# Kernel tuning notes

Hardware: AMD Instinct MI355X
Metric: run time of the kernel (lower is better)

Reference implementation:

```python
import jax, jax.numpy as jnp
import numpy as np

B, L, K, NR, S = 512, 1024, 8, 512, 20  # batch, seq_len, n_matrices, n_rates, alphabet
EXT = 26  # extended alphabet (20 std aa + 6 special), pad of 6 in call()


def _expm(A):
    """Differentiable matrix exponential for small batched matrices (..., n, n).
    Scaling-and-squaring with an order-16 Taylor series (fixed 6 squarings).
    Matches tf.linalg.expm to high accuracy for the small-norm tau*Q here."""
    SQ = 6
    A = A / jnp.asarray(2.0 ** SQ, A.dtype)
    n = A.shape[-1]
    I = jnp.eye(n, dtype=A.dtype)
    P = I + A
    T = A
    for i in range(2, 17):
        T = jnp.matmul(T, A) / i
        P = P + T
    for _ in range(SQ):
        P = jnp.matmul(P, P)
    return P


def setup_inputs() -> dict:
    key = jax.random.key(0)
    k1, k2, k3, k4, k5 = jax.random.split(key, 5)
    return {
        "inputs": jax.random.randint(k1, (B, L), 0, EXT, dtype=jnp.int32),
        "rate_indices": jax.random.randint(k2, (B,), 0, NR, dtype=jnp.int32),
        "tau_kernel": jax.random.normal(k3, (NR,), dtype=jnp.float32),
        "exchangeability_kernel": jax.random.normal(k4, (K, S, S), dtype=jnp.float32),
        "frequencies": jax.random.uniform(k5, (S,), dtype=jnp.float32, minval=0.01, maxval=1.0),
    }


def reference(inputs, rate_indices, tau_kernel, exchangeability_kernel, frequencies):
    b, l = inputs.shape
    mask = inputs < S                                   # (b, L) std-aa mask
    std = jnp.where(mask, inputs, 0)                    # clamp special tokens to 0
    maskf = mask.astype(jnp.float32)[:, :, None, None]  # (b, L, 1, 1)

    # make_R: symmetrize, softplus, zero diagonal
    eye = jnp.eye(S, dtype=jnp.float32)
    R = jax.nn.softplus(0.5 * (exchangeability_kernel + jnp.swapaxes(exchangeability_kernel, -1, -2)))
    R = R * (1.0 - eye)

    # make_rate_matrix: Q = R * pi, subtract row-sum diagonal, normalize by expected rate
    Q = R * frequencies[None, None, :]                  # (k, s, s)
    diag = jnp.sum(Q, axis=-1, keepdims=True)           # (k, s, 1)
    Q = Q - diag * eye
    mue = jnp.sum(frequencies[None, :, None] * diag, axis=-2, keepdims=True)  # (k, 1, 1)
    Q = Q / jnp.maximum(mue, 1e-16)

    # per-sequence evolutionary times
    tau = jax.nn.softplus(tau_kernel)[rate_indices]     # (b,)

    # batched small-matrix expm: (b, k, s, s)
    P = _expm(tau[:, None, None, None] * Q[None])

    # gather ancestral probability rows: (b, L, k, s)
    anc = P[jnp.arange(b)[:, None], :, std, :]
    anc = anc * maskf
    anc = jnp.pad(anc, ((0, 0), (0, 0), (0, 0), (0, EXT - S)))  # pad 20 -> 26
    rest = jax.nn.one_hot(inputs, EXT, dtype=jnp.float32)[:, :, None, :] * (1.0 - maskf)
    anc = anc + rest                                    # (b, L, k, 26)
    return anc.reshape(b, l, -1)                        # (b, L, k*26)
```

## Files before the change

### kernel.cpp

```cpp
#include <hip/hip_runtime.h>
#include <math.h>

#define B    512
#define L    1024
#define K    8
#define NR   512
#define S    20
#define EXT  26
#define SS   (S*S)
#define PD   24
#define PDSQ (PD*PD)
#define ROWF (K*EXT)
#define BROW (L*ROWF)

__device__ __forceinline__ float softplusf(float x) {
    return fmaxf(x, 0.0f) + log1pf(expf(-fabsf(x)));
}

__device__ __forceinline__ void wave_fence() {
    __builtin_amdgcn_wave_barrier();
}

__global__ __launch_bounds__(512, 2) void fused_kernel(
    const int*   __restrict__ inputs,
    const int*   __restrict__ rate_indices,
    const float* __restrict__ tau_kernel,
    const float* __restrict__ exch,
    const float* __restrict__ freq,
    float* __restrict__ out)
{
    __shared__ __align__(16) float M[K][2][PDSQ];
    __shared__ __align__(16) float Row[EXT*ROWF];
    __shared__ int   inp_sh[L];
    __shared__ float diag_sh[K][S];
    __shared__ float mue_sh[K];

    const int b    = blockIdx.x;
    const int t    = threadIdx.x;
    const int w    = t >> 6;
    const int lane = t & 63;
    const int li = lane >> 3, lj = lane & 7;
    const int r0 = 3*li, c0 = 3*lj;

    for (int u = t; u < L; u += 512) inp_sh[u] = inputs[b*L + u];
    for (int e = t; e < EXT*ROWF; e += 512) {
        int row = e / ROWF, c = e - row*ROWF;
        int k = c / EXT, s = c - k*EXT;
        if (row < S) {
            if (s >= S) Row[e] = 0.f;
        } else {
            Row[e] = (s == row) ? 1.f : 0.f;
        }
    }
    float* M0 = &M[w][0][0];
    float* M1 = &M[w][1][0];
    for (int e = lane; e < 2*PDSQ; e += 64) M0[e] = 0.f;
    float tau = softplusf(tau_kernel[rate_indices[b]]);
    wave_fence();

    const float* E = exch + w * SS;
    for (int e = lane; e < SS; e += 64) {
        int r = e / S, c = e - r*S;
        float v = 0.f;
        if (r != c)
            v = softplusf(0.5f * (E[r*S + c] + E[c*S + r])) * freq[c];
        M0[r*PD + c] = v;
    }
    wave_fence();
    if (lane < S) {
        float d = 0.f;
        #pragma unroll
        for (int j = 0; j < S; ++j) d += M0[lane*PD + j];
        diag_sh[w][lane] = d;
    }
    wave_fence();
    if (lane == 0) {
        float m = 0.f;
        #pragma unroll
        for (int s = 0; s < S; ++s) m += freq[s] * diag_sh[w][s];
        mue_sh[w] = fmaxf(m, 1e-16f);
    }
    wave_fence();
    {
        float scale = tau * 0.015625f;
        float mue   = mue_sh[w];
        for (int e = lane; e < SS; e += 64) {
            int r = e / S, c = e - r*S;
            float v = (r == c) ? -diag_sh[w][r] : M0[r*PD + c];
            M0[r*PD + c] = (v / mue) * scale;
        }
    }
    wave_fence();

    float Ac[S][3];
    #pragma unroll
    for (int j = 0; j < S; ++j) {
        #pragma unroll
        for (int d = 0; d < 3; ++d)
            Ac[j][d] = M0[j*PD + c0 + d];
    }

    float P[3][3];
    #pragma unroll
    for (int dr = 0; dr < 3; ++dr)
        #pragma unroll
        for (int dc = 0; dc < 3; ++dc) {
            int r = r0 + dr, c = c0 + dc;
            P[dr][dc] = M0[r*PD + c] + ((r == c && r < S) ? 1.f : 0.f);
        }

    const float* Tc = M0;
    float* Tn = M1;
    #pragma unroll 1
    for (int i = 2; i <= 10; ++i) {
        float C[3][3] = {{0.f,0.f,0.f},{0.f,0.f,0.f},{0.f,0.f,0.f}};
        #pragma unroll
        for (int jc = 0; jc < 5; ++jc) {
            float4 a0 = *(const float4*)&Tc[(r0+0)*PD + 4*jc];
            float4 a1 = *(const float4*)&Tc[(r0+1)*PD + 4*jc];
            float4 a2 = *(const float4*)&Tc[(r0+2)*PD + 4*jc];
            float t0[4] = {a0.x, a0.y, a0.z, a0.w};
            float t1[4] = {a1.x, a1.y, a1.z, a1.w};
            float t2[4] = {a2.x, a2.y, a2.z, a2.w};
            #pragma unroll
            for (int dj = 0; dj < 4; ++dj) {
                int j = 4*jc + dj;
                #pragma unroll
                for (int dc = 0; dc < 3; ++dc) {
                    C[0][dc] = fmaf(t0[dj], Ac[j][dc], C[0][dc]);
                    C[1][dc] = fmaf(t1[dj], Ac[j][dc], C[1][dc]);
                    C[2][dc] = fmaf(t2[dj], Ac[j][dc], C[2][dc]);
                }
            }
        }
        float inv = 1.0f / (float)i;
        #pragma unroll
        for (int dr = 0; dr < 3; ++dr)
            #pragma unroll
            for (int dc = 0; dc < 3; ++dc) {
                C[dr][dc] *= inv;
                P[dr][dc] += C[dr][dc];
                Tn[(r0+dr)*PD + c0 + dc] = C[dr][dc];
            }
        wave_fence();
        float* tmp = (float*)Tc; Tc = Tn; Tn = tmp;
    }

    #pragma unroll 1
    for (int sq = 0; sq < 6; ++sq) {
        #pragma unroll
        for (int dr = 0; dr < 3; ++dr)
            #pragma unroll
            for (int dc = 0; dc < 3; ++dc)
                Tn[(r0+dr)*PD + c0 + dc] = P[dr][dc];
        wave_fence();
        const float* Pb = Tn;
        float C[3][3] = {{0.f,0.f,0.f},{0.f,0.f,0.f},{0.f,0.f,0.f}};
        #pragma unroll
        for (int jc = 0; jc < 5; ++jc) {
            float4 a0 = *(const float4*)&Pb[(r0+0)*PD + 4*jc];
            float4 a1 = *(const float4*)&Pb[(r0+1)*PD + 4*jc];
            float4 a2 = *(const float4*)&Pb[(r0+2)*PD + 4*jc];
            float t0[4] = {a0.x, a0.y, a0.z, a0.w};
            float t1[4] = {a1.x, a1.y, a1.z, a1.w};
            float t2[4] = {a2.x, a2.y, a2.z, a2.w};
            float cb[4][3];
            #pragma unroll
            for (int dj = 0; dj < 4; ++dj)
                #pragma unroll
                for (int dc = 0; dc < 3; ++dc)
                    cb[dj][dc] = Pb[(4*jc + dj)*PD + c0 + dc];
            #pragma unroll
            for (int dj = 0; dj < 4; ++dj)
                #pragma unroll
                for (int dc = 0; dc < 3; ++dc) {
                    C[0][dc] = fmaf(t0[dj], cb[dj][dc], C[0][dc]);
                    C[1][dc] = fmaf(t1[dj], cb[dj][dc], C[1][dc]);
                    C[2][dc] = fmaf(t2[dj], cb[dj][dc], C[2][dc]);
                }
        }
        #pragma unroll
        for (int dr = 0; dr < 3; ++dr)
            #pragma unroll
            for (int dc = 0; dc < 3; ++dc)
                P[dr][dc] = C[dr][dc];
        float* tmp = (float*)Tc; Tc = Tn; Tn = tmp;
        wave_fence();
    }

    #pragma unroll
    for (int dr = 0; dr < 3; ++dr) {
        int r = r0 + dr; if (r >= S) continue;
        #pragma unroll
        for (int dc = 0; dc < 3; ++dc) {
            int c = c0 + dc; if (c >= S) continue;
            Row[r*ROWF + w*EXT + c] = P[dr][dc];
        }
    }
    __syncthreads();

    int l0[13], qq[13];
    {
        int uu = t;
        #pragma unroll
        for (int j = 0; j < 13; ++j) {
            l0[j] = uu / 52;
            qq[j] = uu - l0[j] * 52;
            uu += 512;
        }
    }
    const float4* Row4 = (const float4*)Row;
    float4* out4 = (float4*)out + (size_t)b * (BROW/4);
    #pragma unroll 1
    for (int i = 0; i < 8; ++i) {
        int lbase = i << 7;
        int ubase = t + i * 6656;
        #pragma unroll
        for (int j = 0; j < 13; ++j) {
            int inp = inp_sh[l0[j] + lbase];
            out4[ubase + (j << 9)] = Row4[inp * 52 + qq[j]];
        }
    }
}

extern "C" void kernel_launch(void* const* d_in, const int* in_sizes, int n_in,
                              void* d_out, int out_size, void* d_ws, size_t ws_size,
                              hipStream_t stream) {
    const int*   inputs  = (const int*)  d_in[0];
    const int*   rate_ix = (const int*)  d_in[1];
    const float* tau_k   = (const float*)d_in[2];
    const float* exch    = (const float*)d_in[3];
    const float* freq    = (const float*)d_in[4];
    float* out = (float*)d_out;

    (void)d_ws; (void)ws_size;

    fused_kernel<<<B, 512, 0, stream>>>(inputs, rate_ix, tau_k, exch, freq, out);
}
```

Measured before the change: 478.0 us.

## Split expm and output streaming into two kernels with global LUT and nontemporal stores

The fused kernel becomes two kernels. The first computes the per-batch expm and writes a 26x208 lookup table to workspace. The second kernel runs 2048 blocks of 256 threads, each streaming a quarter of a sequence's output by gathering rows from the global LUT and writing them with nontemporal stores. This is meant to decouple the expm compute from the bandwidth-bound write phase and give the write phase higher occupancy, at the cost of an extra launch and LUT reads that go through L2 instead of LDS.

After: 492.2 us. 3.0% more time.

```diff
diff --git a/kernel.cpp b/kernel.cpp
--- a/kernel.cpp
+++ b/kernel.cpp
@@ -11,7 +11,10 @@
 #define PD   24
 #define PDSQ (PD*PD)
 #define ROWF (K*EXT)
+#define ROWQ ((EXT*ROWF)/4)
 #define BROW (L*ROWF)
+
+typedef float f4 __attribute__((ext_vector_type(4)));
 
 __device__ __forceinline__ float softplusf(float x) {
     return fmaxf(x, 0.0f) + log1pf(expf(-fabsf(x)));
@@ -21,17 +24,15 @@
     __builtin_amdgcn_wave_barrier();
 }
 
-__global__ __launch_bounds__(512, 2) void fused_kernel(
-    const int*   __restrict__ inputs,
+__global__ __launch_bounds__(512, 2) void expm_kernel(
     const int*   __restrict__ rate_indices,
     const float* __restrict__ tau_kernel,
     const float* __restrict__ exch,
     const float* __restrict__ freq,
-    float* __restrict__ out)
+    float*       __restrict__ lut)
 {
     __shared__ __align__(16) float M[K][2][PDSQ];
     __shared__ __align__(16) float Row[EXT*ROWF];
-    __shared__ int   inp_sh[L];
     __shared__ float diag_sh[K][S];
     __shared__ float mue_sh[K];
 
@@ -42,10 +43,10 @@
     const int li = lane >> 3, lj = lane & 7;
     const int r0 = 3*li, c0 = 3*lj;
 
-    for (int u = t; u < L; u += 512) inp_sh[u] = inputs[b*L + u];
     for (int e = t; e < EXT*ROWF; e += 512) {
         int row = e / ROWF, c = e - row*ROWF;
         int k = c / EXT, s = c - k*EXT;
+        (void)k;
         if (row < S) {
             if (s >= S) Row[e] = 0.f;
         } else {
@@ -199,6 +200,25 @@
     }
     __syncthreads();
 
+    f4* dst = (f4*)lut + (size_t)b * ROWQ;
+    const f4* src = (const f4*)Row;
+    for (int e = t; e < ROWQ; e += 512) dst[e] = src[e];
+}
+
+__global__ __launch_bounds__(256, 4) void stream_kernel(
+    const int*   __restrict__ inputs,
+    const float* __restrict__ lut,
+    float*       __restrict__ out)
+{
+    __shared__ int inp_sh[256];
+    const int bid = blockIdx.x;
+    const int b   = bid & (B - 1);
+    const int q   = bid >> 9;
+    const int t   = threadIdx.x;
+
+    inp_sh[t] = inputs[b*L + (q << 8) + t];
+    __syncthreads();
+
     int l0[13], qq[13];
     {
         int uu = t;
@@ -206,19 +226,22 @@
         for (int j = 0; j < 13; ++j) {
             l0[j] = uu / 52;
             qq[j] = uu - l0[j] * 52;
-            uu += 512;
-        }
-    }
-    const float4* Row4 = (const float4*)Row;
-    float4* out4 = (float4*)out + (size_t)b * (BROW/4);
+            uu += 256;
+        }
+    }
+
+    const f4* lut4 = (const f4*)lut + b * ROWQ;
+    f4* out4 = (f4*)out + (size_t)b * (BROW/4) + q * 13312;
+
     #pragma unroll 1
-    for (int i = 0; i < 8; ++i) {
-        int lbase = i << 7;
-        int ubase = t + i * 6656;
+    for (int a = 0; a < 4; ++a) {
+        int lb = a << 6;
+        int ub = t + a * 3328;
         #pragma unroll
         for (int j = 0; j < 13; ++j) {
-            int inp = inp_sh[l0[j] + lbase];
-            out4[ubase + (j << 9)] = Row4[inp * 52 + qq[j]];
+            int inp = inp_sh[l0[j] + lb];
+            f4 v = lut4[inp * 52 + qq[j]];
+            __builtin_nontemporal_store(v, &out4[ub + (j << 8)]);
         }
     }
 }
@@ -232,8 +255,10 @@
     const float* exch    = (const float*)d_in[3];
     const float* freq    = (const float*)d_in[4];
     float* out = (float*)d_out;
-
-    (void)d_ws; (void)ws_size;
-
-    fused_kernel<<<B, 512, 0, stream>>>(inputs, rate_ix, tau_k, exch, freq, out);
-}
+    float* lut = (float*)d_ws;
+
+    (void)in_sizes; (void)n_in; (void)out_size; (void)ws_size;
+
+    expm_kernel<<<B, 512, 0, stream>>>(rate_ix, tau_k, exch, freq, lut);
+    stream_kernel<<<4*B, 256, 0, stream>>>(inputs, lut, out);
+}
```

## Replace Taylor expm with Jacobi eigendecomposition computed once per rate matrix

Applied to the files above, without the earlier changes.

Each rate matrix is symmetrised with sqrt(pi) and diagonalised once per matrix by a cyclic Jacobi kernel that runs 8 sweeps. The per-sequence expm then becomes X·diag(exp(tau·lambda))·Y, which is a single 20x20 product instead of 9 Taylor terms plus 6 squarings. This removes most of the per-block matrix-multiply work ahead of the output write. In exchange it adds a second serial launch with only 8 single-wave blocks. Accuracy now depends on how well the fixed number of Jacobi sweeps converges.

Result: slower. 771.9 us (+61.5%).

```diff
diff --git a/kernel.cpp b/kernel.cpp
--- a/kernel.cpp
+++ b/kernel.cpp
@@ -8,10 +8,11 @@
 #define S    20
 #define EXT  26
 #define SS   (S*S)
-#define PD   24
-#define PDSQ (PD*PD)
 #define ROWF (K*EXT)
 #define BROW (L*ROWF)
+#define KSTR 840
+
+typedef float f4 __attribute__((ext_vector_type(4)));
 
 __device__ __forceinline__ float softplusf(float x) {
     return fmaxf(x, 0.0f) + log1pf(expf(-fabsf(x)));
@@ -21,19 +22,135 @@
     __builtin_amdgcn_wave_barrier();
 }
 
-__global__ __launch_bounds__(512, 2) void fused_kernel(
+__global__ __launch_bounds__(64, 1) void eigen_kernel(
+    const float* __restrict__ exch,
+    const float* __restrict__ freq,
+    float*       __restrict__ XYL)
+{
+    __shared__ float Am[20*21];
+    __shared__ float Um[20*21];
+    __shared__ float sq[20];
+    __shared__ float dd[20];
+    __shared__ float inv_mue_sh;
+    __shared__ float cs_c[10], cs_s[10];
+    __shared__ int   pr[10], qr[10];
+
+    const int k    = blockIdx.x;
+    const int lane = threadIdx.x;
+    const float* E = exch + k * SS;
+
+    if (lane < 20) sq[lane] = sqrtf(freq[lane]);
+    wave_fence();
+
+    for (int e = lane; e < 400; e += 64) {
+        int r = e / 20, c = e - r*20;
+        float v = 0.f;
+        if (r != c)
+            v = softplusf(0.5f * (E[r*20 + c] + E[c*20 + r])) * sq[r] * sq[c];
+        Am[r*21 + c] = v;
+        Um[r*21 + c] = (r == c) ? 1.f : 0.f;
+    }
+    wave_fence();
+    if (lane < 20) {
+        float sacc = 0.f;
+        #pragma unroll
+        for (int j = 0; j < 20; ++j) sacc += Am[lane*21 + j] * sq[j];
+        dd[lane] = sacc / sq[lane];
+    }
+    wave_fence();
+    if (lane == 0) {
+        float m = 0.f;
+        #pragma unroll
+        for (int r = 0; r < 20; ++r) m += sq[r] * sq[r] * dd[r];
+        inv_mue_sh = 1.f / fmaxf(m, 1e-16f);
+    }
+    wave_fence();
+    {
+        float inv_mue = inv_mue_sh;
+        for (int e = lane; e < 400; e += 64) {
+            int r = e / 20, c = e - r*20;
+            Am[r*21 + c] = (r == c) ? (-dd[r] * inv_mue) : (Am[r*21 + c] * inv_mue);
+        }
+    }
+    wave_fence();
+
+    #pragma unroll 1
+    for (int sweep = 0; sweep < 8; ++sweep) {
+        #pragma unroll 1
+        for (int rr = 0; rr < 19; ++rr) {
+            if (lane < 10) {
+                int p, q;
+                if (lane == 0) { p = 19; q = rr; }
+                else { p = (rr + lane) % 19; q = (rr + 19 - lane) % 19; }
+                float apq = Am[p*21 + q];
+                float c = 1.f, s = 0.f;
+                if (fabsf(apq) > 1e-25f) {
+                    float theta = (Am[q*21 + q] - Am[p*21 + p]) / (2.f * apq);
+                    float tt = copysignf(1.f / (fabsf(theta) + sqrtf(theta*theta + 1.f)), theta);
+                    c = 1.f / sqrtf(tt*tt + 1.f);
+                    s = tt * c;
+                }
+                cs_c[lane] = c; cs_s[lane] = s; pr[lane] = p; qr[lane] = q;
+            }
+            wave_fence();
+            for (int t4 = lane; t4 < 400; t4 += 64) {
+                int m = t4 / 40, rem = t4 - m*40;
+                int p = pr[m], q = qr[m];
+                float c = cs_c[m], s = cs_s[m];
+                if (rem < 20) {
+                    int j = rem;
+                    float ap = Am[p*21 + j], aq = Am[q*21 + j];
+                    Am[p*21 + j] = c*ap - s*aq;
+                    Am[q*21 + j] = s*ap + c*aq;
+                } else {
+                    int i = rem - 20;
+                    float up = Um[i*21 + p], uq = Um[i*21 + q];
+                    Um[i*21 + p] = c*up - s*uq;
+                    Um[i*21 + q] = s*up + c*uq;
+                }
+            }
+            wave_fence();
+            for (int t4 = lane; t4 < 200; t4 += 64) {
+                int m = t4 / 20, i = t4 - m*20;
+                int p = pr[m], q = qr[m];
+                float c = cs_c[m], s = cs_s[m];
+                float ap = Am[i*21 + p], aq = Am[i*21 + q];
+                Am[i*21 + p] = c*ap - s*aq;
+                Am[i*21 + q] = s*ap + c*aq;
+            }
+            wave_fence();
+        }
+    }
+
+    float* O = XYL + k * KSTR;
+    for (int e = lane; e < KSTR; e += 64) {
+        float v = 0.f;
+        if (e < 400) {
+            int r = e / 20, c = e - r*20;
+            v = Um[r*21 + c] / sq[r];
+        } else if (e < 800) {
+            int i = e - 400; int j = i / 20, c = i - j*20;
+            v = Um[c*21 + j] * sq[c];
+        } else if (e < 820) {
+            int j = e - 800;
+            v = Am[j*21 + j];
+        }
+        O[e] = v;
+    }
+}
+
+__global__ __launch_bounds__(512, 2) void fused2_kernel(
     const int*   __restrict__ inputs,
     const int*   __restrict__ rate_indices,
     const float* __restrict__ tau_kernel,
-    const float* __restrict__ exch,
-    const float* __restrict__ freq,
-    float* __restrict__ out)
+    const float* __restrict__ XYL,
+    float*       __restrict__ out)
 {
-    __shared__ __align__(16) float M[K][2][PDSQ];
+    __shared__ __align__(16) float Xs[K][400];
+    __shared__ float Ys[K][400];
+    __shared__ float lam_sh[K][20];
     __shared__ __align__(16) float Row[EXT*ROWF];
-    __shared__ int   inp_sh[L];
-    __shared__ float diag_sh[K][S];
-    __shared__ float mue_sh[K];
+    __shared__ int inp_sh[L];
 
     const int b    = blockIdx.x;
     const int t    = threadIdx.x;
@@ -45,80 +162,46 @@
     for (int u = t; u < L; u += 512) inp_sh[u] = inputs[b*L + u];
     for (int e = t; e < EXT*ROWF; e += 512) {
         int row = e / ROWF, c = e - row*ROWF;
-        int k = c / EXT, s = c - k*EXT;
+        int kk = c / EXT, s = c - kk*EXT;
+        (void)kk;
         if (row < S) {
             if (s >= S) Row[e] = 0.f;
         } else {
             Row[e] = (s == row) ? 1.f : 0.f;
         }
     }
-    float* M0 = &M[w][0][0];
-    float* M1 = &M[w][1][0];
-    for (int e = lane; e < 2*PDSQ; e += 64) M0[e] = 0.f;
+    for (int e = t; e < K*KSTR; e += 512) {
+        int k = e / KSTR, rem = e - k*KSTR;
+        float v = XYL[e];
+        if (rem < 400)      Xs[k][rem] = v;
+        else if (rem < 800) Ys[k][rem - 400] = v;
+        else if (rem < 820) lam_sh[k][rem - 800] = v;
+    }
     float tau = softplusf(tau_kernel[rate_indices[b]]);
-    wave_fence();
-
-    const float* E = exch + w * SS;
-    for (int e = lane; e < SS; e += 64) {
-        int r = e / S, c = e - r*S;
-        float v = 0.f;
-        if (r != c)
-            v = softplusf(0.5f * (E[r*S + c] + E[c*S + r])) * freq[c];
-        M0[r*PD + c] = v;
-    }
-    wave_fence();
-    if (lane < S) {
-        float d = 0.f;
-        #pragma unroll
-        for (int j = 0; j < S; ++j) d += M0[lane*PD + j];
-        diag_sh[w][lane] = d;
-    }
-    wave_fence();
-    if (lane == 0) {
-        float m = 0.f;
-        #pragma unroll
-        for (int s = 0; s < S; ++s) m += freq[s] * diag_sh[w][s];
-        mue_sh[w] = fmaxf(m, 1e-16f);
-    }
-    wave_fence();
-    {
-        float scale = tau * 0.015625f;
-        float mue   = mue_sh[w];
-        for (int e = lane; e < SS; e += 64) {
-            int r = e / S, c = e - r*S;
-            float v = (r == c) ? -diag_sh[w][r] : M0[r*PD + c];
-            M0[r*PD + c] = (v / mue) * scale;
-        }
-    }
-    wave_fence();
-
-    float Ac[S][3];
+    __syncthreads();
+
+    float Ye[S][3];
     #pragma unroll
     for (int j = 0; j < S; ++j) {
-        #pragma unroll
-        for (int d = 0; d < 3; ++d)
-            Ac[j][d] = M0[j*PD + c0 + d];
-    }
-
-    float P[3][3];
-    #pragma unroll
-    for (int dr = 0; dr < 3; ++dr)
+        float ej = __expf(tau * lam_sh[w][j]);
         #pragma unroll
         for (int dc = 0; dc < 3; ++dc) {
-            int r = r0 + dr, c = c0 + dc;
-            P[dr][dc] = M0[r*PD + c] + ((r == c && r < S) ? 1.f : 0.f);
-        }
-
-    const float* Tc = M0;
-    float* Tn = M1;
-    #pragma unroll 1
-    for (int i = 2; i <= 10; ++i) {
-        float C[3][3] = {{0.f,0.f,0.f},{0.f,0.f,0.f},{0.f,0.f,0.f}};
+            int c = c0 + dc;
+            Ye[j][dc] = (c < S) ? ej * Ys[w][j*20 + c] : 0.f;
+        }
+    }
+
+    float C[3][3] = {{0.f,0.f,0.f},{0.f,0.f,0.f},{0.f,0.f,0.f}};
+    {
+        const float* Xw = &Xs[w][0];
+        const bool v0 = (r0 + 0) < S;
+        const bool v1 = (r0 + 1) < S;
+        const bool v2 = (r0 + 2) < S;
         #pragma unroll
         for (int jc = 0; jc < 5; ++jc) {
-            float4 a0 = *(const float4*)&Tc[(r0+0)*PD + 4*jc];
-            float4 a1 = *(const float4*)&Tc[(r0+1)*PD + 4*jc];
-            float4 a2 = *(const float4*)&Tc[(r0+2)*PD + 4*jc];
+            float4 a0 = v0 ? *(const float4*)&Xw[(r0+0)*20 + 4*jc] : make_float4(0,0,0,0);
+            float4 a1 = v1 ? *(const float4*)&Xw[(r0+1)*20 + 4*jc] : make_float4(0,0,0,0);
+            float4 a2 = v2 ? *(const float4*)&Xw[(r0+2)*20 + 4*jc] : make_float4(0,0,0,0);
             float t0[4] = {a0.x, a0.y, a0.z, a0.w};
             float t1[4] = {a1.x, a1.y, a1.z, a1.w};
             float t2[4] = {a2.x, a2.y, a2.z, a2.w};
@@ -127,65 +210,12 @@
                 int j = 4*jc + dj;
                 #pragma unroll
                 for (int dc = 0; dc < 3; ++dc) {
-                    C[0][dc] = fmaf(t0[dj], Ac[j][dc], C[0][dc]);
-                    C[1][dc] = fmaf(t1[dj], Ac[j][dc], C[1][dc]);
-                    C[2][dc] = fmaf(t2[dj], Ac[j][dc], C[2][dc]);
+                    C[0][dc] = fmaf(t0[dj], Ye[j][dc], C[0][dc]);
+                    C[1][dc] = fmaf(t1[dj], Ye[j][dc], C[1][dc]);
+                    C[2][dc] = fmaf(t2[dj], Ye[j][dc], C[2][dc]);
                 }
             }
         }
-        float inv = 1.0f / (float)i;
-        #pragma unroll
-        for (int dr = 0; dr < 3; ++dr)
-            #pragma unroll
-            for (int dc = 0; dc < 3; ++dc) {
-                C[dr][dc] *= inv;
-                P[dr][dc] += C[dr][dc];
-                Tn[(r0+dr)*PD + c0 + dc] = C[dr][dc];
-            }
-        wave_fence();
-        float* tmp = (float*)Tc; Tc = Tn; Tn = tmp;
-    }
-
-    #pragma unroll 1
-    for (int sq = 0; sq < 6; ++sq) {
-        #pragma unroll
-        for (int dr = 0; dr < 3; ++dr)
-            #pragma unroll
-            for (int dc = 0; dc < 3; ++dc)
-                Tn[(r0+dr)*PD + c0 + dc] = P[dr][dc];
-        wave_fence();
-        const float* Pb = Tn;
-        float C[3][3] = {{0.f,0.f,0.f},{0.f,0.f,0.f},{0.f,0.f,0.f}};
-        #pragma unroll
-        for (int jc = 0; jc < 5; ++jc) {
-            float4 a0 = *(const float4*)&Pb[(r0+0)*PD + 4*jc];
-            float4 a1 = *(const float4*)&Pb[(r0+1)*PD + 4*jc];
-            float4 a2 = *(const float4*)&Pb[(r0+2)*PD + 4*jc];
-            float t0[4] = {a0.x, a0.y, a0.z, a0.w};
-            float t1[4] = {a1.x, a1.y, a1.z, a1.w};
-            float t2[4] = {a2.x, a2.y, a2.z, a2.w};
-            float cb[4][3];
-            #pragma unroll
-            for (int dj = 0; dj < 4; ++dj)
-                #pragma unroll
-                for (int dc = 0; dc < 3; ++dc)
-                    cb[dj][dc] = Pb[(4*jc + dj)*PD + c0 + dc];
-            #pragma unroll
-            for (int dj = 0; dj < 4; ++dj)
-                #pragma unroll
-                for (int dc = 0; dc < 3; ++dc) {
-                    C[0][dc] = fmaf(t0[dj], cb[dj][dc], C[0][dc]);
-                    C[1][dc] = fmaf(t1[dj], cb[dj][dc], C[1][dc]);
-                    C[2][dc] = fmaf(t2[dj], cb[dj][dc], C[2][dc]);
-                }
-        }
-        #pragma unroll
-        for (int dr = 0; dr < 3; ++dr)
-            #pragma unroll
-            for (int dc = 0; dc < 3; ++dc)
-                P[dr][dc] = C[dr][dc];
-        float* tmp = (float*)Tc; Tc = Tn; Tn = tmp;
-        wave_fence();
     }
 
     #pragma unroll
@@ -194,7 +224,7 @@
         #pragma unroll
         for (int dc = 0; dc < 3; ++dc) {
             int c = c0 + dc; if (c >= S) continue;
-            Row[r*ROWF + w*EXT + c] = P[dr][dc];
+            Row[r*ROWF + w*EXT + c] = C[dr][dc];
         }
     }
     __syncthreads();
@@ -209,8 +239,8 @@
             uu += 512;
         }
     }
-    const float4* Row4 = (const float4*)Row;
-    float4* out4 = (float4*)out + (size_t)b * (BROW/4);
+    const f4* Row4 = (const f4*)Row;
+    f4* out4 = (f4*)out + (size_t)b * (BROW/4);
     #pragma unroll 1
     for (int i = 0; i < 8; ++i) {
         int lbase = i << 7;
@@ -232,8 +262,10 @@
     const float* exch    = (const float*)d_in[3];
     const float* freq    = (const float*)d_in[4];
     float* out = (float*)d_out;
-
-    (void)d_ws; (void)ws_size;
-
-    fused_kernel<<<B, 512, 0, stream>>>(inputs, rate_ix, tau_k, exch, freq, out);
-}
+    float* xyl = (float*)d_ws;
+
+    (void)in_sizes; (void)n_in; (void)out_size; (void)ws_size;
+
+    eigen_kernel<<<K, 64, 0, stream>>>(exch, freq, xyl);
+    fused2_kernel<<<B, 512, 0, stream>>>(inputs, rate_ix, tau_k, xyl, out);
+}
```
